# Optimization experiments

Hardware: AMD Instinct MI355X
Metric: run time of the kernel (lower is better)

Reference implementation:

```python
import jax, jax.numpy as jnp
import numpy as np

N = 131072  # total sentences
D = 768     # relation/sentence embedding dim
B = 16384   # number of bags (scopes)
C = 53      # n_class (NYT10 relations)


def setup_inputs() -> dict:
    key = jax.random.key(0)
    k1, k2, k3, k4, k5 = jax.random.split(key, 5)
    x = jax.random.normal(k1, (N, D), dtype=jnp.float32)
    label = jax.random.randint(k2, (N,), 0, C)              # per-sentence bag label
    segment_ids = jnp.sort(jax.random.randint(k3, (N,), 0, B))  # sorted -> contiguous scopes
    rel_weight = jax.random.normal(k4, (C, D), dtype=jnp.float32) * 0.05  # relation_matrix.weight
    bias = jax.random.normal(k5, (C,), dtype=jnp.float32)
    return {"x": x, "label": label, "segment_ids": segment_ids,
            "rel_weight": rel_weight, "bias": bias}


def reference(x, label, segment_ids, rel_weight, bias):
    # _attention_train_logit: <x_i, relation_matrix[label_i]>  -> [N]
    att = jnp.sum(x * rel_weight[label], axis=1)
    # per-bag (segment) stable softmax over sentences in each scope
    seg_max = jax.ops.segment_max(att, segment_ids, num_segments=B)      # [B]
    e = jnp.exp(att - seg_max[segment_ids])                              # [N]
    denom = jax.ops.segment_sum(e, segment_ids, num_segments=B)         # [B]
    # softmax-weighted pooling: sum_i softmax_i * x_i per bag
    num = jax.ops.segment_sum(e[:, None] * x, segment_ids, num_segments=B)  # [B, D]
    repre = num / jnp.where(denom == 0, 1.0, denom)[:, None]
    # get_logits (dropout=0.0 -> identity)
    logits = repre @ rel_weight.T + bias                                 # [B, C]
    return logits
```

## Files before the change

### kernel.cpp

```cpp
#include <hip/hip_runtime.h>
#include <math.h>

#define DN  768
#define NC  53
#define NCP 64
#define NKS 24
#define MB  256

typedef __attribute__((ext_vector_type(8))) __bf16 bf16x8;
typedef __attribute__((ext_vector_type(8))) short short8v;
typedef __attribute__((ext_vector_type(4))) float f32x4;

static __device__ __forceinline__ unsigned short f2bf(float f) {
    unsigned int u = __builtin_bit_cast(unsigned int, f);
    u = (u + 0x7FFFu + ((u >> 16) & 1u)) >> 16;
    return (unsigned short)u;
}

__global__ void prep_wb(const float* __restrict__ w, unsigned short* __restrict__ wb) {
    int i = blockIdx.x * 256 + threadIdx.x;
    if (i >= NKS * 4 * 64 * 8) return;
    const int e    = i & 7;
    const int lane = (i >> 3) & 63;
    const int ct   = (i >> 9) & 3;
    const int ks   = i >> 11;
    const int cls  = ct * 16 + (lane & 15);
    const int k    = ks * 32 + ((lane >> 4) << 3) + e;
    wb[i] = (cls < NC) ? f2bf(w[cls * DN + k]) : (unsigned short)0;
}

__global__ void offs_kernel(const int* __restrict__ seg, int* __restrict__ offs,
                            int N, int B) {
    int i = blockIdx.x * blockDim.x + threadIdx.x;
    if (i >= N) return;
    int cur  = seg[i];
    int prev = (i == 0) ? -1 : seg[i - 1];
    for (int b = prev + 1; b <= cur; ++b) offs[b] = i;
    if (i == N - 1)
        for (int b = cur + 1; b <= B; ++b) offs[b] = N;
}

#define ISSUE(buf, ks)                                                         \
    {                                                                          \
        _Pragma("unroll")                                                      \
        for (int f = 0; f < 4; ++f) {                                          \
            const float* ap = a0 + (size_t)f * 16 * DN + (ks) * 32;            \
            la[buf][f * 2]     = *(const float4*)(ap);                         \
            la[buf][f * 2 + 1] = *(const float4*)(ap + 4);                     \
        }                                                                      \
        _Pragma("unroll")                                                      \
        for (int ct = 0; ct < 4; ++ct)                                         \
            lb[buf][ct] = *(const short8v*)(wb + (((ks) * 4 + ct) * 64 + lane) * 8); \
    }

__global__ __launch_bounds__(256) void gemm_y2(
    const float* __restrict__ x,
    const unsigned short* __restrict__ wb,
    float* __restrict__ y)
{
    const int lane = threadIdx.x & 63;
    const int wv   = threadIdx.x >> 6;
    const int r16  = lane & 15;
    const int kg   = lane >> 4;
    const long row0 = (long)blockIdx.x * MB + wv * 64;

    f32x4 acc[4][4];
    #pragma unroll
    for (int f = 0; f < 4; ++f)
        #pragma unroll
        for (int ct = 0; ct < 4; ++ct)
            acc[f][ct] = (f32x4){0.f, 0.f, 0.f, 0.f};

    const float* a0 = x + (row0 + r16) * DN + kg * 8;

    float4  la[2][8];
    short8v lb[2][4];
    ISSUE(0, 0)

    #pragma unroll
    for (int ks = 0; ks < NKS; ++ks) {
        const int cur = ks & 1, nxt = cur ^ 1;
        if (ks + 1 < NKS) ISSUE(nxt, ks + 1)

        short8v a8[4];
        #pragma unroll
        for (int f = 0; f < 4; ++f) {
            const float4 u0 = la[cur][f * 2], u1 = la[cur][f * 2 + 1];
            short8v t;
            t[0] = (short)f2bf(u0.x); t[1] = (short)f2bf(u0.y);
            t[2] = (short)f2bf(u0.z); t[3] = (short)f2bf(u0.w);
            t[4] = (short)f2bf(u1.x); t[5] = (short)f2bf(u1.y);
            t[6] = (short)f2bf(u1.z); t[7] = (short)f2bf(u1.w);
            a8[f] = t;
        }
        #pragma unroll
        for (int ct = 0; ct < 4; ++ct)
            #pragma unroll
            for (int f = 0; f < 4; ++f)
                acc[f][ct] = __builtin_amdgcn_mfma_f32_16x16x32_bf16(
                    __builtin_bit_cast(bf16x8, a8[f]),
                    __builtin_bit_cast(bf16x8, lb[cur][ct]), acc[f][ct], 0, 0, 0);
    }

    #pragma unroll
    for (int f = 0; f < 4; ++f)
        #pragma unroll
        for (int ct = 0; ct < 4; ++ct) {
            const long row = row0 + f * 16 + kg * 4;
            #pragma unroll
            for (int r = 0; r < 4; ++r)
                y[(row + r) * NCP + ct * 16 + r16] = acc[f][ct][r];
        }
}

__global__ __launch_bounds__(256) void pool_kernel(
    const float* __restrict__ y,
    const int*   __restrict__ label,
    const int*   __restrict__ offs,
    const float* __restrict__ bias,
    float*       __restrict__ out,
    int Btot)
{
    __shared__ float s_e[4][64];
    const int wv   = threadIdx.x >> 6;
    const int lane = threadIdx.x & 63;
    const int bag  = blockIdx.x * 4 + wv;
    if (bag >= Btot) return;
    const int s = offs[bag], e = offs[bag + 1];

    float m = -INFINITY, den = 0.f, facc = 0.f;
    for (int j0 = s; j0 < e; j0 += 64) {
        const int j = j0 + lane;
        float a = -INFINITY;
        if (j < e) a = y[(size_t)j * NCP + label[j]];
        float cm = a;
        #pragma unroll
        for (int off = 1; off < 64; off <<= 1) cm = fmaxf(cm, __shfl_xor(cm, off));
        const float nm = fmaxf(m, cm);
        const float sc = __expf(m - nm);
        const float ej = __expf(a - nm);
        float cd = ej;
        #pragma unroll
        for (int off = 1; off < 64; off <<= 1) cd += __shfl_xor(cd, off);
        den = den * sc + cd;
        s_e[wv][lane] = ej;
        const int cnt = min(64, e - j0);
        float f0 = 0.f, f1 = 0.f, f2 = 0.f, f3 = 0.f;
        int t = 0;
        for (; t + 4 <= cnt; t += 4) {
            f0 += s_e[wv][t]     * y[(size_t)(j0 + t)     * NCP + lane];
            f1 += s_e[wv][t + 1] * y[(size_t)(j0 + t + 1) * NCP + lane];
            f2 += s_e[wv][t + 2] * y[(size_t)(j0 + t + 2) * NCP + lane];
            f3 += s_e[wv][t + 3] * y[(size_t)(j0 + t + 3) * NCP + lane];
        }
        for (; t < cnt; ++t)
            f0 += s_e[wv][t] * y[(size_t)(j0 + t) * NCP + lane];
        facc = facc * sc + ((f0 + f1) + (f2 + f3));
        m = nm;
    }
    if (lane < NC) {
        const float inv = (den == 0.f) ? 0.f : 1.f / den;
        out[(size_t)bag * NC + lane] = facc * inv + bias[lane];
    }
}

extern "C" void kernel_launch(void* const* d_in, const int* in_sizes, int n_in,
                              void* d_out, int out_size, void* d_ws, size_t ws_size,
                              hipStream_t stream)
{
    const float* x     = (const float*)d_in[0];
    const int*   label = (const int*)  d_in[1];
    const int*   seg   = (const int*)  d_in[2];
    const float* w     = (const float*)d_in[3];
    const float* bias  = (const float*)d_in[4];
    float*       out   = (float*)d_out;

    const int N = in_sizes[0] / DN;
    const int B = out_size / NC;

    unsigned short* wb   = (unsigned short*)d_ws;
    int*            offs = (int*)((char*)d_ws + 131072);
    float*          y    = (float*)((char*)d_ws + 1048576);

    hipLaunchKernelGGL(prep_wb, dim3(192), dim3(256), 0, stream, w, wb);
    hipLaunchKernelGGL(offs_kernel, dim3((N + 255) / 256), dim3(256), 0, stream,
                       seg, offs, N, B);
    hipLaunchKernelGGL(gemm_y2, dim3(N / MB), dim3(256), 0, stream, x, wb, y);
    hipLaunchKernelGGL(pool_kernel, dim3((B + 3) / 4), dim3(256), 0, stream,
                       y, label, offs, bias, out, B);
}
```

Measured before the change: 119.0 us.

## Store GEMM output as bf16, precompute attention logits, merge prep kernels

The GEMM kernel now writes the per-sentence class scores as bf16 instead of fp32, which halves the intermediate buffer traffic. It also stages the fp32 tile in shared memory so each row's attention logit (the score at its label) can be extracted and stored in a separate array. The two preparation kernels are merged into one launch to cut launch overhead. The pooling kernel reads the precomputed logits and the bf16 scores. This trades some precision in the pooled sum for less memory traffic, and adds a large shared-memory footprint that may reduce GEMM occupancy.

```diff
diff --git a/kernel.cpp b/kernel.cpp
--- a/kernel.cpp
+++ b/kernel.cpp
@@ -6,6 +6,7 @@
 #define NCP 64
 #define NKS 24
 #define MB  256
+#define YTS 66
 
 typedef __attribute__((ext_vector_type(8))) __bf16 bf16x8;
 typedef __attribute__((ext_vector_type(8))) short short8v;
@@ -16,28 +17,35 @@
     u = (u + 0x7FFFu + ((u >> 16) & 1u)) >> 16;
     return (unsigned short)u;
 }
-
-__global__ void prep_wb(const float* __restrict__ w, unsigned short* __restrict__ wb) {
-    int i = blockIdx.x * 256 + threadIdx.x;
-    if (i >= NKS * 4 * 64 * 8) return;
-    const int e    = i & 7;
-    const int lane = (i >> 3) & 63;
-    const int ct   = (i >> 9) & 3;
-    const int ks   = i >> 11;
-    const int cls  = ct * 16 + (lane & 15);
-    const int k    = ks * 32 + ((lane >> 4) << 3) + e;
-    wb[i] = (cls < NC) ? f2bf(w[cls * DN + k]) : (unsigned short)0;
-}
-
-__global__ void offs_kernel(const int* __restrict__ seg, int* __restrict__ offs,
+static __device__ __forceinline__ float bf2f(unsigned short h) {
+    unsigned int u = ((unsigned int)h) << 16;
+    return __builtin_bit_cast(float, u);
+}
+
+__global__ void prep_kernel(const float* __restrict__ w,
+                            const int*   __restrict__ seg,
+                            unsigned short* __restrict__ wb,
+                            int* __restrict__ offs,
                             int N, int B) {
-    int i = blockIdx.x * blockDim.x + threadIdx.x;
-    if (i >= N) return;
-    int cur  = seg[i];
-    int prev = (i == 0) ? -1 : seg[i - 1];
-    for (int b = prev + 1; b <= cur; ++b) offs[b] = i;
-    if (i == N - 1)
-        for (int b = cur + 1; b <= B; ++b) offs[b] = N;
+    const int bid = blockIdx.x;
+    if (bid < 192) {
+        int i = bid * 256 + threadIdx.x;
+        const int e    = i & 7;
+        const int lane = (i >> 3) & 63;
+        const int ct   = (i >> 9) & 3;
+        const int ks   = i >> 11;
+        const int cls  = ct * 16 + (lane & 15);
+        const int k    = ks * 32 + ((lane >> 4) << 3) + e;
+        wb[i] = (cls < NC) ? f2bf(w[cls * DN + k]) : (unsigned short)0;
+    } else {
+        int i = (bid - 192) * 256 + threadIdx.x;
+        if (i >= N) return;
+        int cur  = seg[i];
+        int prev = (i == 0) ? -1 : seg[i - 1];
+        for (int b = prev + 1; b <= cur; ++b) offs[b] = i;
+        if (i == N - 1)
+            for (int b = cur + 1; b <= B; ++b) offs[b] = N;
+    }
 }
 
 #define ISSUE(buf, ks)                                                         \
@@ -53,11 +61,15 @@
             lb[buf][ct] = *(const short8v*)(wb + (((ks) * 4 + ct) * 64 + lane) * 8); \
     }
 
-__global__ __launch_bounds__(256) void gemm_y2(
+__global__ __launch_bounds__(256) void gemm_y3(
     const float* __restrict__ x,
+    const int*   __restrict__ label,
     const unsigned short* __restrict__ wb,
-    float* __restrict__ y)
+    unsigned short* __restrict__ yb,
+    float* __restrict__ att)
 {
+    __shared__ float yt[4][64 * YTS];
+
     const int lane = threadIdx.x & 63;
     const int wv   = threadIdx.x >> 6;
     const int r16  = lane & 15;
@@ -102,20 +114,29 @@
                     __builtin_bit_cast(bf16x8, lb[cur][ct]), acc[f][ct], 0, 0, 0);
     }
 
+    float* myt = yt[wv];
     #pragma unroll
     for (int f = 0; f < 4; ++f)
         #pragma unroll
         for (int ct = 0; ct < 4; ++ct) {
-            const long row = row0 + f * 16 + kg * 4;
+            const int rl = f * 16 + kg * 4;
             #pragma unroll
-            for (int r = 0; r < 4; ++r)
-                y[(row + r) * NCP + ct * 16 + r16] = acc[f][ct][r];
+            for (int r = 0; r < 4; ++r) {
+                const float v = acc[f][ct][r];
+                myt[(rl + r) * YTS + ct * 16 + r16] = v;
+                yb[(row0 + rl + r) * NCP + ct * 16 + r16] = f2bf(v);
+            }
         }
+    {
+        const long grow = row0 + lane;
+        const int  lab  = label[grow];
+        att[grow] = myt[lane * YTS + lab];
+    }
 }
 
 __global__ __launch_bounds__(256) void pool_kernel(
-    const float* __restrict__ y,
-    const int*   __restrict__ label,
+    const unsigned short* __restrict__ yb,
+    const float* __restrict__ att,
     const int*   __restrict__ offs,
     const float* __restrict__ bias,
     float*       __restrict__ out,
@@ -131,14 +152,13 @@
     float m = -INFINITY, den = 0.f, facc = 0.f;
     for (int j0 = s; j0 < e; j0 += 64) {
         const int j = j0 + lane;
-        float a = -INFINITY;
-        if (j < e) a = y[(size_t)j * NCP + label[j]];
+        float a = (j < e) ? att[j] : -INFINITY;
         float cm = a;
         #pragma unroll
         for (int off = 1; off < 64; off <<= 1) cm = fmaxf(cm, __shfl_xor(cm, off));
         const float nm = fmaxf(m, cm);
         const float sc = __expf(m - nm);
-        const float ej = __expf(a - nm);
+        const float ej = (j < e) ? __expf(a - nm) : 0.f;
         float cd = ej;
         #pragma unroll
         for (int off = 1; off < 64; off <<= 1) cd += __shfl_xor(cd, off);
@@ -148,13 +168,13 @@
         float f0 = 0.f, f1 = 0.f, f2 = 0.f, f3 = 0.f;
         int t = 0;
         for (; t + 4 <= cnt; t += 4) {
-            f0 += s_e[wv][t]     * y[(size_t)(j0 + t)     * NCP + lane];
-            f1 += s_e[wv][t + 1] * y[(size_t)(j0 + t + 1) * NCP + lane];
-            f2 += s_e[wv][t + 2] * y[(size_t)(j0 + t + 2) * NCP + lane];
-            f3 += s_e[wv][t + 3] * y[(size_t)(j0 + t + 3) * NCP + lane];
+            f0 += s_e[wv][t]     * bf2f(yb[(size_t)(j0 + t)     * NCP + lane]);
+            f1 += s_e[wv][t + 1] * bf2f(yb[(size_t)(j0 + t + 1) * NCP + lane]);
+            f2 += s_e[wv][t + 2] * bf2f(yb[(size_t)(j0 + t + 2) * NCP + lane]);
+            f3 += s_e[wv][t + 3] * bf2f(yb[(size_t)(j0 + t + 3) * NCP + lane]);
         }
         for (; t < cnt; ++t)
-            f0 += s_e[wv][t] * y[(size_t)(j0 + t) * NCP + lane];
+            f0 += s_e[wv][t] * bf2f(yb[(size_t)(j0 + t) * NCP + lane]);
         facc = facc * sc + ((f0 + f1) + (f2 + f3));
         m = nm;
     }
@@ -180,12 +200,13 @@
 
     unsigned short* wb   = (unsigned short*)d_ws;
     int*            offs = (int*)((char*)d_ws + 131072);
-    float*          y    = (float*)((char*)d_ws + 1048576);
-
-    hipLaunchKernelGGL(prep_wb, dim3(192), dim3(256), 0, stream, w, wb);
-    hipLaunchKernelGGL(offs_kernel, dim3((N + 255) / 256), dim3(256), 0, stream,
-                       seg, offs, N, B);
-    hipLaunchKernelGGL(gemm_y2, dim3(N / MB), dim3(256), 0, stream, x, wb, y);
+    float*          att  = (float*)((char*)d_ws + 1048576);
+    unsigned short* yb   = (unsigned short*)((char*)d_ws + 2097152);
+
+    hipLaunchKernelGGL(prep_kernel, dim3(192 + (N + 255) / 256), dim3(256), 0, stream,
+                       w, seg, wb, offs, N, B);
+    hipLaunchKernelGGL(gemm_y3, dim3(N / MB), dim3(256), 0, stream,
+                       x, label, wb, yb, att);
     hipLaunchKernelGGL(pool_kernel, dim3((B + 3) / 4), dim3(256), 0, stream,
-                       y, label, offs, bias, out, B);
-}
+                       yb, att, offs, bias, out, B);
+}
```

New measurement: 113.5 us. 1.05x faster.
